# Performance work log

Measured on AMD Instinct MI355X. Metric: run time of the kernel, lower is better.

Reference implementation:

```python
import jax, jax.numpy as jnp
import numpy as np

H, L, NB = 128, 2048, 64  # features, seq len, half state size (conj-symmetric N=128)


def _forward(u, x_re, x_im, Lambda_re, Lambda_im, B_re, B_im, C_re, C_im, D, d):
    Lam = (Lambda_re + 1j * Lambda_im).astype(jnp.complex64)   # (H, NB) discrete diag A
    B = (B_re + 1j * B_im).astype(jnp.complex64)               # (H, NB)
    C = (C_re + 1j * C_im).astype(jnp.complex64)               # (H, NB)
    x0 = (x_re + 1j * x_im).astype(jnp.complex64)              # (H, NB) initial state
    Hn, Ln = u.shape
    # scan elements (A_t, b_t, d_t); identity element (1, x0, False) prepended at t=0
    A = jnp.concatenate([jnp.ones((Hn, 1, NB), jnp.complex64),
                         jnp.broadcast_to(Lam[:, None, :], (Hn, Ln, NB))], axis=1)
    b = jnp.concatenate([x0[:, None, :],
                         B[:, None, :] * u[:, :, None].astype(jnp.complex64)], axis=1)
    dd = jnp.concatenate([jnp.zeros((1,), bool), d.astype(bool)])[None, :, None]  # (1, L+1, 1)

    def combine(lhs, rhs):
        # reset-aware associative combine: if right done-flag set, drop left contribution
        A_i, b_i, c_i = lhs
        A_j, b_j, c_j = rhs
        return (jnp.where(c_j, A_j, A_j * A_i),
                jnp.where(c_j, b_j, A_j * b_i + b_j),
                jnp.logical_or(c_i, c_j))

    _, xs, _ = jax.lax.associative_scan(combine, (A, b, dd), axis=1)
    xs = xs[:, 1:]                                             # (H, L, NB) hidden states
    # conj symmetry: y_t = 2*Re(C @ x_t) + D * u_t
    y = 2.0 * jnp.real(jnp.einsum('hn,hln->hl', C, xs)) + D[:, None] * u
    return y, xs[:, -1]


def setup_inputs():
    key = jax.random.key(0)
    ks = jax.random.split(key, 8)
    # stable ZOH-discretized HiPPO-like diagonal system (mirrors LSSL-f init)
    dts = jnp.logspace(-3.0, -1.0, H)                          # (H,) per-feature timescales
    k = jnp.arange(NB, dtype=jnp.float32)
    lam_c = -0.5 + 1j * jnp.pi * (2.0 * k + 1.0)               # (NB,) continuous poles
    lam_d = jnp.exp(dts[:, None] * lam_c[None, :]).astype(jnp.complex64)  # (H, NB), |.|<1
    Bc = ((jax.random.normal(ks[0], (NB,)) + 1j * jax.random.normal(ks[1], (NB,)))
          / jnp.sqrt(2.0 * NB)).astype(jnp.complex64)
    Bd = (((lam_d - 1.0) / lam_c[None, :]) * Bc[None, :]).astype(jnp.complex64)  # (H, NB)
    C = ((jax.random.normal(ks[2], (H, NB)) + 1j * jax.random.normal(ks[3], (H, NB)))
         / jnp.sqrt(float(NB))).astype(jnp.complex64)
    return {
        "u": jax.random.normal(ks[4], (H, L), jnp.float32),
        "x_re": jnp.zeros((H, NB), jnp.float32),
        "x_im": jnp.zeros((H, NB), jnp.float32),
        "Lambda_re": jnp.real(lam_d).astype(jnp.float32),
        "Lambda_im": jnp.imag(lam_d).astype(jnp.float32),
        "B_re": jnp.real(Bd).astype(jnp.float32),
        "B_im": jnp.imag(Bd).astype(jnp.float32),
        "C_re": jnp.real(C).astype(jnp.float32),
        "C_im": jnp.imag(C).astype(jnp.float32),
        "D": jax.random.normal(ks[5], (H,), jnp.float32),
        "d": jax.random.bernoulli(ks[6], 0.01, (L,)),
    }


def reference(u, x_re, x_im, Lambda_re, Lambda_im, B_re, B_im, C_re, C_im, D, d):
    return _forward(u, x_re, x_im, Lambda_re, Lambda_im, B_re, B_im, C_re, C_im, D, d)
```

## Files before the change

### kernel.cpp

```cpp
#include <hip/hip_runtime.h>

#define Hn 128
#define Ln 2048
#define NBn 64
#define K 64
#define G 32
#define PITCH 65


__global__ __launch_bounds__(64) void phase1_local(
    const float* __restrict__ u,
    const float* __restrict__ Lre,  const float* __restrict__ Lim,
    const float* __restrict__ Bre,  const float* __restrict__ Bim,
    const float* __restrict__ Cre,  const float* __restrict__ Cim,
    const float* __restrict__ Dv,   const int* __restrict__ dflag,
    float* __restrict__ out,
    float4* __restrict__ Sum)
{
    __shared__ float g_s[K * PITCH];
    __shared__ float u_s[K];

    const int g = blockIdx.x, h = blockIdx.y, n = threadIdx.x;
    const int hn = h * NBn + n;
    const int l0 = g * K;

    const float lre = Lre[hn], lim = Lim[hn];
    const float br  = Bre[hn], bi  = Bim[hn];
    const float cr  = Cre[hn], ci  = Cim[hn];
    const float Dh  = Dv[h];
    const float cbr2 = 2.f * (cr * br - ci * bi);
    const float cbi2 = 2.f * (cr * bi + ci * br);

    u_s[n] = u[h * Ln + l0 + n];
    const unsigned long long m = __ballot(dflag[l0 + n] != 0);
    __syncthreads();

    float wr = 0.f, wi = 0.f;
    if (m == 0ull) {
        #pragma unroll
        for (int k = 0; k < K; ++k) {
            const float uk = u_s[k];
            const float nr = fmaf(lre, wr, fmaf(-lim, wi, cbr2 * uk));
            const float ni = fmaf(lre, wi, fmaf( lim, wr, cbi2 * uk));
            wr = nr; wi = ni;
            g_s[k * PITCH + n] = wr;
        }
    } else {
        #pragma unroll
        for (int k = 0; k < K; ++k) {
            const bool  rs  = (m >> k) & 1ull;
            const float lrk = rs ? 0.f : lre;
            const float lik = rs ? 0.f : lim;
            const float uk  = u_s[k];
            const float nr = fmaf(lrk, wr, fmaf(-lik, wi, cbr2 * uk));
            const float ni = fmaf(lrk, wi, fmaf( lik, wr, cbi2 * uk));
            wr = nr; wi = ni;
            g_s[k * PITCH + n] = wr;
        }
    }
    __syncthreads();

    const float* row = g_s + n * PITCH;
    float a0 = 0.f, a1 = 0.f, a2 = 0.f, a3 = 0.f;
    #pragma unroll
    for (int k = 0; k < NBn; k += 4) {
        a0 += row[k + 0]; a1 += row[k + 1];
        a2 += row[k + 2]; a3 += row[k + 3];
    }
    out[h * Ln + l0 + n] = (a0 + a1) + (a2 + a3) + Dh * u_s[n];

    float pr = lre, pi = lim;
    #pragma unroll
    for (int it = 0; it < 6; ++it) {
        const float sr2 = pr * pr - pi * pi;
        const float si2 = 2.f * pr * pi;
        pr = sr2; pi = si2;
    }
    if (m) { pr = 0.f; pi = 0.f; }
    Sum[(h * G + g) * NBn + n] = make_float4(pr, pi, wr, wi);
}

__global__ __launch_bounds__(64) void phase2_combine(
    const float* __restrict__ x_re, const float* __restrict__ x_im,
    const float* __restrict__ Cre,  const float* __restrict__ Cim,
    const float4* __restrict__ Sum,
    float2* __restrict__ Sin,
    float* __restrict__ out)
{
    const int h = blockIdx.x, n = threadIdx.x;
    const int hn = h * NBn + n;
    const float cr = Cre[hn], ci = Cim[hn];
    const float x0r = x_re[hn], x0i = x_im[hn];
    float sre = 2.f * (cr * x0r - ci * x0i);
    float sim = 2.f * (cr * x0i + ci * x0r);
    #pragma unroll
    for (int g = 0; g < G; ++g) {
        const int idx = (h * G + g) * NBn + n;
        const float4 s = Sum[idx];
        Sin[idx] = make_float2(sre, sim);
        const float nr = fmaf(s.x, sre, fmaf(-s.y, sim, s.z));
        const float ni = fmaf(s.x, sim, fmaf( s.y, sre, s.w));
        sre = nr; sim = ni;
    }
    const float c2r = 2.f * cr, c2i = 2.f * ci;
    const float inv = 1.f / (c2r * c2r + c2i * c2i);
    float* xlast = out + Hn * Ln;
    xlast[2 * hn + 0] = (sre * c2r + sim * c2i) * inv;
    xlast[2 * hn + 1] = (sim * c2r - sre * c2i) * inv;
}

__global__ __launch_bounds__(64) void phase3_fixup(
    const float* __restrict__ Lre, const float* __restrict__ Lim,
    const int* __restrict__ dflag,
    const float2* __restrict__ Sin,
    float* __restrict__ out)
{
    __shared__ float g_s[K * PITCH];

    const int g = blockIdx.x, h = blockIdx.y, n = threadIdx.x;
    const int hn = h * NBn + n;
    const int l0 = g * K;

    const float2 s = Sin[(h * G + g) * NBn + n];
    const float lre = Lre[hn], lim = Lim[hn];

    const unsigned long long bal = __ballot(dflag[l0 + n] != 0);
    const int kr = bal ? (__ffsll((long long)bal) - 1) : K;

    const float l2r = lre * lre - lim * lim;
    const float l2i = 2.f * lre * lim;

    float tAr = fmaf(lre, s.x, -lim * s.y);
    float tAi = fmaf(lre, s.y,  lim * s.x);
    float tBr = fmaf(l2r, s.x, -l2i * s.y);
    float tBi = fmaf(l2r, s.y,  l2i * s.x);
    g_s[0 * PITCH + n] = tAr;
    g_s[1 * PITCH + n] = tBr;
    #pragma unroll
    for (int k = 2; k < K; k += 2) {
        const float nAr = fmaf(l2r, tAr, -l2i * tAi);
        const float nAi = fmaf(l2r, tAi,  l2i * tAr);
        tAr = nAr; tAi = nAi;
        g_s[k * PITCH + n] = tAr;
        const float nBr = fmaf(l2r, tBr, -l2i * tBi);
        const float nBi = fmaf(l2r, tBi,  l2i * tBr);
        tBr = nBr; tBi = nBi;
        g_s[(k + 1) * PITCH + n] = tBr;
    }
    __syncthreads();

    const float* row = g_s + n * PITCH;
    float a0 = 0.f, a1 = 0.f, a2 = 0.f, a3 = 0.f;
    #pragma unroll
    for (int k = 0; k < NBn; k += 4) {
        a0 += row[k + 0]; a1 += row[k + 1];
        a2 += row[k + 2]; a3 += row[k + 3];
    }
    if (n < kr)
        out[h * Ln + l0 + n] += (a0 + a1) + (a2 + a3);
}

extern "C" void kernel_launch(void* const* d_in, const int* in_sizes, int n_in,
                              void* d_out, int out_size, void* d_ws, size_t ws_size,
                              hipStream_t stream) {
    const float* u    = (const float*)d_in[0];
    const float* x_re = (const float*)d_in[1];
    const float* x_im = (const float*)d_in[2];
    const float* Lre  = (const float*)d_in[3];
    const float* Lim  = (const float*)d_in[4];
    const float* Bre  = (const float*)d_in[5];
    const float* Bim  = (const float*)d_in[6];
    const float* Cre  = (const float*)d_in[7];
    const float* Cim  = (const float*)d_in[8];
    const float* Dv   = (const float*)d_in[9];
    const int*   dfl  = (const int*)d_in[10];
    float* out = (float*)d_out;

    const int HGN = Hn * G * NBn;
    float4* Sum = (float4*)d_ws;
    float2* Sin = (float2*)(Sum + HGN);

    dim3 grid(G, Hn);
    phase1_local<<<grid, 64, 0, stream>>>(u, Lre, Lim, Bre, Bim, Cre, Cim,
                                          Dv, dfl, out, Sum);
    phase2_combine<<<Hn, 64, 0, stream>>>(x_re, x_im, Cre, Cim, Sum, Sin, out);
    phase3_fixup<<<grid, 64, 0, stream>>>(Lre, Lim, dfl, Sin, out);
}
```

Baseline: 88.58 us.

## Fuse three scan phases into one cooperative kernel with grid syncs

Merges the local-scan, carry-combine and fixup kernels into a single persistent cooperative kernel that loops over tiles and separates the phases with grid.sync(). The aim is to remove two kernel-launch boundaries and their drain/ramp overhead. In exchange it caps parallelism at the occupancy-limited grid, the combine phase runs on only 128 blocks while the others wait, and grid-wide barriers add their own cost. It falls back to the three-kernel path if cooperative launch is unavailable.

After: 337.0 us. +280.4%, slower.

```diff
diff --git a/kernel.cpp b/kernel.cpp
--- a/kernel.cpp
+++ b/kernel.cpp
@@ -1,4 +1,7 @@
 #include <hip/hip_runtime.h>
+#include <hip/hip_cooperative_groups.h>
+
+namespace cg = cooperative_groups;
 
 #define Hn 128
 #define Ln 2048
@@ -6,7 +9,165 @@
 #define K 64
 #define G 32
 #define PITCH 65
-
+#define NTILES (Hn * G)
+
+
+__global__ __launch_bounds__(64, 2) void fused_scan(
+    const float* __restrict__ u,
+    const float* __restrict__ x_re, const float* __restrict__ x_im,
+    const float* __restrict__ Lre,  const float* __restrict__ Lim,
+    const float* __restrict__ Bre,  const float* __restrict__ Bim,
+    const float* __restrict__ Cre,  const float* __restrict__ Cim,
+    const float* __restrict__ Dv,   const int* __restrict__ dflag,
+    float* __restrict__ out,
+    float4* __restrict__ Sum,
+    float2* __restrict__ Sin)
+{
+    __shared__ float g_s[K * PITCH];
+    __shared__ float u_s[K];
+
+    cg::grid_group grid = cg::this_grid();
+    const int n    = threadIdx.x;
+    const int nblk = gridDim.x;
+
+    for (int tile = blockIdx.x; tile < NTILES; tile += nblk) {
+        const int h  = tile >> 5;
+        const int g  = tile & 31;
+        const int hn = h * NBn + n;
+        const int l0 = g * K;
+
+        __syncthreads();
+
+        const float lre = Lre[hn], lim = Lim[hn];
+        const float br  = Bre[hn], bi  = Bim[hn];
+        const float cr  = Cre[hn], ci  = Cim[hn];
+        const float Dh  = Dv[h];
+        const float cbr2 = 2.f * (cr * br - ci * bi);
+        const float cbi2 = 2.f * (cr * bi + ci * br);
+
+        const float un = u[h * Ln + l0 + n];
+        u_s[n] = un;
+        const unsigned long long m = __ballot(dflag[l0 + n] != 0);
+        __syncthreads();
+
+        float wr = 0.f, wi = 0.f;
+        if (m == 0ull) {
+            #pragma unroll
+            for (int k = 0; k < K; ++k) {
+                const float uk = u_s[k];
+                const float nr = fmaf(lre, wr, fmaf(-lim, wi, cbr2 * uk));
+                const float ni = fmaf(lre, wi, fmaf( lim, wr, cbi2 * uk));
+                wr = nr; wi = ni;
+                g_s[k * PITCH + n] = wr;
+            }
+        } else {
+            #pragma unroll
+            for (int k = 0; k < K; ++k) {
+                const bool  rs  = (m >> k) & 1ull;
+                const float lrk = rs ? 0.f : lre;
+                const float lik = rs ? 0.f : lim;
+                const float uk  = u_s[k];
+                const float nr = fmaf(lrk, wr, fmaf(-lik, wi, cbr2 * uk));
+                const float ni = fmaf(lrk, wi, fmaf( lik, wr, cbi2 * uk));
+                wr = nr; wi = ni;
+                g_s[k * PITCH + n] = wr;
+            }
+        }
+        __syncthreads();
+
+        const float* row = g_s + n * PITCH;
+        float a0 = 0.f, a1 = 0.f, a2 = 0.f, a3 = 0.f;
+        #pragma unroll
+        for (int k = 0; k < NBn; k += 4) {
+            a0 += row[k + 0]; a1 += row[k + 1];
+            a2 += row[k + 2]; a3 += row[k + 3];
+        }
+        out[h * Ln + l0 + n] = (a0 + a1) + (a2 + a3) + Dh * un;
+
+        float pr = lre, pi = lim;
+        #pragma unroll
+        for (int it = 0; it < 6; ++it) {
+            const float sr2 = pr * pr - pi * pi;
+            const float si2 = 2.f * pr * pi;
+            pr = sr2; pi = si2;
+        }
+        if (m) { pr = 0.f; pi = 0.f; }
+        Sum[(h * G + g) * NBn + n] = make_float4(pr, pi, wr, wi);
+    }
+
+    grid.sync();
+
+    for (int h2 = blockIdx.x; h2 < Hn; h2 += nblk) {
+        const int hn2 = h2 * NBn + n;
+        const float cr2 = Cre[hn2], ci2 = Cim[hn2];
+        const float x0r = x_re[hn2], x0i = x_im[hn2];
+        float sre = 2.f * (cr2 * x0r - ci2 * x0i);
+        float sim = 2.f * (cr2 * x0i + ci2 * x0r);
+        #pragma unroll
+        for (int gg = 0; gg < G; ++gg) {
+            const int idx = (h2 * G + gg) * NBn + n;
+            const float4 s = Sum[idx];
+            Sin[idx] = make_float2(sre, sim);
+            const float nr = fmaf(s.x, sre, fmaf(-s.y, sim, s.z));
+            const float ni = fmaf(s.x, sim, fmaf( s.y, sre, s.w));
+            sre = nr; sim = ni;
+        }
+        const float c2r = 2.f * cr2, c2i = 2.f * ci2;
+        const float inv = 1.f / (c2r * c2r + c2i * c2i);
+        float* xlast = out + Hn * Ln;
+        xlast[2 * hn2 + 0] = (sre * c2r + sim * c2i) * inv;
+        xlast[2 * hn2 + 1] = (sim * c2r - sre * c2i) * inv;
+    }
+
+    grid.sync();
+
+    for (int tile = blockIdx.x; tile < NTILES; tile += nblk) {
+        const int h  = tile >> 5;
+        const int g  = tile & 31;
+        const int hn = h * NBn + n;
+        const int l0 = g * K;
+
+        __syncthreads();
+
+        const float lre = Lre[hn], lim = Lim[hn];
+        const float2 s = Sin[(h * G + g) * NBn + n];
+
+        const unsigned long long bal = __ballot(dflag[l0 + n] != 0);
+        const int kr = bal ? (__ffsll((long long)bal) - 1) : K;
+
+        const float l2r = fmaf(lre, lre, -lim * lim);
+        const float l2i = 2.f * lre * lim;
+
+        float tAr = fmaf(lre, s.x, -lim * s.y);
+        float tAi = fmaf(lre, s.y,  lim * s.x);
+        float tBr = fmaf(l2r, s.x, -l2i * s.y);
+        float tBi = fmaf(l2r, s.y,  l2i * s.x);
+        g_s[0 * PITCH + n] = tAr;
+        g_s[1 * PITCH + n] = tBr;
+        #pragma unroll
+        for (int k = 2; k < K; k += 2) {
+            const float nAr = fmaf(l2r, tAr, -l2i * tAi);
+            const float nAi = fmaf(l2r, tAi,  l2i * tAr);
+            tAr = nAr; tAi = nAi;
+            g_s[k * PITCH + n] = tAr;
+            const float nBr = fmaf(l2r, tBr, -l2i * tBi);
+            const float nBi = fmaf(l2r, tBi,  l2i * tBr);
+            tBr = nBr; tBi = nBi;
+            g_s[(k + 1) * PITCH + n] = tBr;
+        }
+        __syncthreads();
+
+        const float* row = g_s + n * PITCH;
+        float a0 = 0.f, a1 = 0.f, a2 = 0.f, a3 = 0.f;
+        #pragma unroll
+        for (int k = 0; k < NBn; k += 4) {
+            a0 += row[k + 0]; a1 += row[k + 1];
+            a2 += row[k + 2]; a3 += row[k + 3];
+        }
+        if (n < kr)
+            out[h * Ln + l0 + n] += (a0 + a1) + (a2 + a3);
+    }
+}
 
 __global__ __launch_bounds__(64) void phase1_local(
     const float* __restrict__ u,
@@ -163,6 +324,7 @@
 extern "C" void kernel_launch(void* const* d_in, const int* in_sizes, int n_in,
                               void* d_out, int out_size, void* d_ws, size_t ws_size,
                               hipStream_t stream) {
+    (void)in_sizes; (void)n_in; (void)out_size; (void)ws_size;
     const float* u    = (const float*)d_in[0];
     const float* x_re = (const float*)d_in[1];
     const float* x_im = (const float*)d_in[2];
@@ -180,6 +342,37 @@
     float4* Sum = (float4*)d_ws;
     float2* Sin = (float2*)(Sum + HGN);
 
+    static int g_nblk = -2;
+    if (g_nblk == -2) {
+        int dev = 0, coop = 0, cus = 0, occ = 0;
+        if (hipGetDevice(&dev) == hipSuccess &&
+            hipDeviceGetAttribute(&coop, hipDeviceAttributeCooperativeLaunch, dev) == hipSuccess &&
+            coop != 0 &&
+            hipDeviceGetAttribute(&cus, hipDeviceAttributeMultiprocessorCount, dev) == hipSuccess &&
+            cus > 0 &&
+            hipOccupancyMaxActiveBlocksPerMultiprocessor(&occ, (const void*)fused_scan, 64, 0) == hipSuccess &&
+            occ >= 1) {
+            long cap = (long)occ * (long)cus;
+            g_nblk = (int)(cap < 2048 ? cap : 2048);
+            if (g_nblk < Hn) g_nblk = -1;
+        } else {
+            g_nblk = -1;
+        }
+    }
+
+    if (g_nblk > 0) {
+        void* args[] = {
+            (void*)&u, (void*)&x_re, (void*)&x_im, (void*)&Lre, (void*)&Lim,
+            (void*)&Bre, (void*)&Bim, (void*)&Cre, (void*)&Cim, (void*)&Dv,
+            (void*)&dfl, (void*)&out, (void*)&Sum, (void*)&Sin
+        };
+        hipError_t err = hipLaunchCooperativeKernel((const void*)fused_scan,
+                                                    dim3(g_nblk), dim3(64),
+                                                    args, 0, stream);
+        if (err == hipSuccess) return;
+        g_nblk = -1;
+    }
+
     dim3 grid(G, Hn);
     phase1_local<<<grid, 64, 0, stream>>>(u, Lre, Lim, Bre, Bim, Cre, Cim,
                                           Dv, dfl, out, Sum);
```

## Fuse chunk-carry combine into fixup kernel with redundant per-block prefix

Applied to the files above, without the earlier changes.

Merges the serial carry-propagation kernel into the fixup kernel. Each (chunk, feature) block now recomputes the prefix over all 32 chunk summaries itself and keeps the carry-in for its own chunk, and only the last chunk writes the final state. This removes one kernel launch, the Sin workspace round-trip, and the low-parallelism 128-block serial pass. In exchange every block redundantly reads all 32 summaries, which adds 32x more reads of Sum, mostly served from cache.

Result: slower. 95.40 us (+7.7%).

```diff
diff --git a/kernel.cpp b/kernel.cpp
--- a/kernel.cpp
+++ b/kernel.cpp
@@ -80,39 +80,12 @@
     Sum[(h * G + g) * NBn + n] = make_float4(pr, pi, wr, wi);
 }
 
-__global__ __launch_bounds__(64) void phase2_combine(
+__global__ __launch_bounds__(64) void phase23_fused(
     const float* __restrict__ x_re, const float* __restrict__ x_im,
     const float* __restrict__ Cre,  const float* __restrict__ Cim,
+    const float* __restrict__ Lre,  const float* __restrict__ Lim,
+    const int* __restrict__ dflag,
     const float4* __restrict__ Sum,
-    float2* __restrict__ Sin,
-    float* __restrict__ out)
-{
-    const int h = blockIdx.x, n = threadIdx.x;
-    const int hn = h * NBn + n;
-    const float cr = Cre[hn], ci = Cim[hn];
-    const float x0r = x_re[hn], x0i = x_im[hn];
-    float sre = 2.f * (cr * x0r - ci * x0i);
-    float sim = 2.f * (cr * x0i + ci * x0r);
-    #pragma unroll
-    for (int g = 0; g < G; ++g) {
-        const int idx = (h * G + g) * NBn + n;
-        const float4 s = Sum[idx];
-        Sin[idx] = make_float2(sre, sim);
-        const float nr = fmaf(s.x, sre, fmaf(-s.y, sim, s.z));
-        const float ni = fmaf(s.x, sim, fmaf( s.y, sre, s.w));
-        sre = nr; sim = ni;
-    }
-    const float c2r = 2.f * cr, c2i = 2.f * ci;
-    const float inv = 1.f / (c2r * c2r + c2i * c2i);
-    float* xlast = out + Hn * Ln;
-    xlast[2 * hn + 0] = (sre * c2r + sim * c2i) * inv;
-    xlast[2 * hn + 1] = (sim * c2r - sre * c2i) * inv;
-}
-
-__global__ __launch_bounds__(64) void phase3_fixup(
-    const float* __restrict__ Lre, const float* __restrict__ Lim,
-    const int* __restrict__ dflag,
-    const float2* __restrict__ Sin,
     float* __restrict__ out)
 {
     __shared__ float g_s[K * PITCH];
@@ -121,7 +94,27 @@
     const int hn = h * NBn + n;
     const int l0 = g * K;
 
-    const float2 s = Sin[(h * G + g) * NBn + n];
+    const float cr = Cre[hn], ci = Cim[hn];
+    const float x0r = x_re[hn], x0i = x_im[hn];
+    float sre = 2.f * (cr * x0r - ci * x0i);
+    float sim = 2.f * (cr * x0i + ci * x0r);
+    float wir = sre, wii = sim;
+    #pragma unroll
+    for (int gg = 0; gg < G; ++gg) {
+        const float4 s = Sum[(h * G + gg) * NBn + n];
+        if (gg == g) { wir = sre; wii = sim; }
+        const float nr = fmaf(s.x, sre, fmaf(-s.y, sim, s.z));
+        const float ni = fmaf(s.x, sim, fmaf( s.y, sre, s.w));
+        sre = nr; sim = ni;
+    }
+    if (g == G - 1) {
+        const float c2r = 2.f * cr, c2i = 2.f * ci;
+        const float inv = 1.f / (c2r * c2r + c2i * c2i);
+        float* xlast = out + Hn * Ln;
+        xlast[2 * hn + 0] = (sre * c2r + sim * c2i) * inv;
+        xlast[2 * hn + 1] = (sim * c2r - sre * c2i) * inv;
+    }
+
     const float lre = Lre[hn], lim = Lim[hn];
 
     const unsigned long long bal = __ballot(dflag[l0 + n] != 0);
@@ -130,10 +123,10 @@
     const float l2r = lre * lre - lim * lim;
     const float l2i = 2.f * lre * lim;
 
-    float tAr = fmaf(lre, s.x, -lim * s.y);
-    float tAi = fmaf(lre, s.y,  lim * s.x);
-    float tBr = fmaf(l2r, s.x, -l2i * s.y);
-    float tBi = fmaf(l2r, s.y,  l2i * s.x);
+    float tAr = fmaf(lre, wir, -lim * wii);
+    float tAi = fmaf(lre, wii,  lim * wir);
+    float tBr = fmaf(l2r, wir, -l2i * wii);
+    float tBi = fmaf(l2r, wii,  l2i * wir);
     g_s[0 * PITCH + n] = tAr;
     g_s[1 * PITCH + n] = tBr;
     #pragma unroll
@@ -163,6 +156,7 @@
 extern "C" void kernel_launch(void* const* d_in, const int* in_sizes, int n_in,
                               void* d_out, int out_size, void* d_ws, size_t ws_size,
                               hipStream_t stream) {
+    (void)in_sizes; (void)n_in; (void)out_size; (void)ws_size;
     const float* u    = (const float*)d_in[0];
     const float* x_re = (const float*)d_in[1];
     const float* x_im = (const float*)d_in[2];
@@ -176,13 +170,11 @@
     const int*   dfl  = (const int*)d_in[10];
     float* out = (float*)d_out;
 
-    const int HGN = Hn * G * NBn;
     float4* Sum = (float4*)d_ws;
-    float2* Sin = (float2*)(Sum + HGN);
 
     dim3 grid(G, Hn);
     phase1_local<<<grid, 64, 0, stream>>>(u, Lre, Lim, Bre, Bim, Cre, Cim,
                                           Dv, dfl, out, Sum);
-    phase2_combine<<<Hn, 64, 0, stream>>>(x_re, x_im, Cre, Cim, Sum, Sin, out);
-    phase3_fixup<<<grid, 64, 0, stream>>>(Lre, Lim, dfl, Sin, out);
+    phase23_fused<<<grid, 64, 0, stream>>>(x_re, x_im, Cre, Cim, Lre, Lim,
+                                           dfl, Sum, out);
 }
```
